# Performance work log

Hardware: AMD Instinct MI355X
Metric: run time of the kernel (lower is better)

## Reference

```python
import jax, jax.numpy as jnp
import numpy as np

WIN = 16
HEADS = 4


def _window_partition(x, win):
    B, H, W, C = x.shape
    x = x.reshape(B, H // win, win, W // win, win, C)
    x = x.transpose(0, 1, 3, 2, 4, 5)
    return x.reshape(-1, win * win, C)


def _reverse_window_partition(x, win, H, W):
    N, _, C = x.shape
    x = x.reshape(-1, H // win, W // win, win, win, C)
    x = x.transpose(0, 1, 3, 2, 4, 5)
    return x.reshape(-1, H, W, C)


def setup_inputs() -> dict:
    key = jax.random.key(0)
    ks = jax.random.split(key, 7)
    B, H, W, C = 2, 256, 256, 96
    s = 0.02
    return {
        "x": jax.random.normal(ks[0], (B, H, W, C), jnp.float32),
        "qkv_w": jax.random.normal(ks[1], (C, 3 * C), jnp.float32) * s,
        "qkv_b": jax.random.normal(ks[2], (3 * C,), jnp.float32) * s,
        "pe_w": jax.random.normal(ks[3], (3, 3, 1, C), jnp.float32) * s,  # depthwise HWIO
        "pe_b": jax.random.normal(ks[4], (C,), jnp.float32) * s,
        "out_w": jax.random.normal(ks[5], (C, C), jnp.float32) * s,
        "out_b": jax.random.normal(ks[6], (C,), jnp.float32) * s,
    }


def reference(x, qkv_w, qkv_b, pe_w, pe_b, out_w, out_b):
    B, H, W, C = x.shape
    win, heads = WIN, HEADS
    hd = C // heads

    z = _window_partition(x, win)
    N, S, _ = z.shape

    qkv = z @ qkv_w + qkv_b                       # (N, S, 3C)
    # headify then chunk(3): each head's 3*hd channels split into q,k,v
    qkv = qkv.reshape(N, S, heads, 3, hd).transpose(0, 2, 3, 1, 4)  # (N, h, 3, S, hd)
    q, k, v = qkv[:, :, 0], qkv[:, :, 1], qkv[:, :, 2]

    # Locally-enhanced PE: depthwise 3x3 conv on de-headified v
    v_img = v.transpose(0, 2, 1, 3).reshape(N, win, win, C)  # NHWC
    lepe = jax.lax.conv_general_dilated(
        v_img, pe_w, (1, 1), 'SAME',
        dimension_numbers=('NHWC', 'HWIO', 'NHWC'),
        feature_group_count=C) + pe_b
    lepe = lepe.reshape(N, S, heads, hd).transpose(0, 2, 1, 3)  # (N, h, S, hd)

    # per-window SDPA (default scale 1/sqrt(hd))
    scale = 1.0 / jnp.sqrt(jnp.asarray(hd, x.dtype))
    attn = jax.nn.softmax(jnp.einsum('nhsd,nhtd->nhst', q, k) * scale, axis=-1)
    o = jnp.einsum('nhst,nhtd->nhsd', attn, v) + lepe

    o = o.transpose(0, 2, 1, 3).reshape(N, S, C)
    o = _reverse_window_partition(o, win, H, W)   # (B, H, W, C)
    return o @ out_w + out_b
```

## Files before the change

### kernel.cpp

```cpp
#include <hip/hip_runtime.h>


typedef __attribute__((ext_vector_type(8))) short bf16x8;
typedef __attribute__((ext_vector_type(4))) float f32x4;

#define MFMA(a, b, c) __builtin_amdgcn_mfma_f32_16x16x32_bf16(a, b, c, 0, 0, 0)

#if __has_builtin(__builtin_amdgcn_exp2f)
#define EXP2F(x) __builtin_amdgcn_exp2f(x)
#else
#define EXP2F(x) exp2f(x)
#endif

#define SCALE2 (0.20412414523193154f * 1.4426950408889634f)

#define OFF_WT   0u
#define OFF_B2   55296u
#define OFF_WTO  56448u
#define OFF_Q    75904u
#define OFF_K    25241728u
#define OFF_VT   50407552u

__device__ __forceinline__ unsigned short f2bf(float f) {
    union { float f; unsigned int u; } v; v.f = f;
    unsigned int u = v.u;
    return (unsigned short)((u + 0x7FFFu + ((u >> 16) & 1u)) >> 16);
}
__device__ __forceinline__ float bf2f(unsigned short h) {
    union { unsigned int u; float f; } v; v.u = ((unsigned int)h) << 16;
    return v.f;
}
__device__ __forceinline__ unsigned int pk2bf(float a, float b) {
#if __has_builtin(__builtin_amdgcn_cvt_pk_bf16_f32)
    auto p = __builtin_amdgcn_cvt_pk_bf16_f32(a, b);
    union { decltype(p) v; unsigned int u; } cv; cv.v = p;
    return cv.u;
#else
    return (unsigned int)f2bf(a) | ((unsigned int)f2bf(b) << 16);
#endif
}
__device__ __forceinline__ float frcp(float x) {
#if __has_builtin(__builtin_amdgcn_rcpf)
    return __builtin_amdgcn_rcpf(x);
#else
    return 1.0f / x;
#endif
}

__global__ void prep_kernel(const float* __restrict__ qkv_w,
                            const float* __restrict__ qkv_b,
                            const float* __restrict__ out_w,
                            unsigned short* __restrict__ wt,
                            float* __restrict__ b2,
                            unsigned short* __restrict__ wto) {
    const int stride = gridDim.x * 256;
    int i0 = blockIdx.x * 256 + threadIdx.x;
    for (int i = i0; i < 288 * 96; i += stride) {
        const int c = i / 96, k = i % 96;
        float v = qkv_w[k * 288 + c];
        if ((c % 72) < 24) v *= SCALE2;
        wt[i] = f2bf(v);
    }
    for (int i = i0; i < 288; i += stride) {
        float v = qkv_b[i];
        if ((i % 72) < 24) v *= SCALE2;
        b2[i] = v;
    }
    for (int i = i0; i < 96 * 96; i += stride) {
        const int c = i / 96, k = i % 96;
        wto[i] = f2bf(out_w[k * 96 + c]);
    }
}

__launch_bounds__(256, 4)
__global__ void qkv_kernel(const float* __restrict__ x,
                           const unsigned short* __restrict__ wt,
                           const float* __restrict__ b2,
                           unsigned short* __restrict__ Qb,
                           unsigned short* __restrict__ Kb,
                           unsigned short* __restrict__ VTb) {
    __shared__ unsigned short z[128 * 104];
    const int blk = blockIdx.x;
    const int n = blk >> 1, half = blk & 1;
    const int T0 = half << 7;
    const int tid = threadIdx.x;
    const int bW = n >> 8, hy = (n >> 4) & 15, wx = n & 15;

    for (int i = tid; i < 128 * 24; i += 256) {
        const int tl = i / 24, c4 = i % 24;
        const int tok = T0 + tl;
        const int y = tok >> 4, xx = tok & 15;
        const size_t row = (size_t)((bW * 256 + hy * 16 + y) * 256 + wx * 16 + xx);
        const float4 v = *(const float4*)(x + row * 96 + c4 * 4);
        uint2 pk; pk.x = pk2bf(v.x, v.y); pk.y = pk2bf(v.z, v.w);
        *(uint2*)&z[tl * 104 + c4 * 4] = pk;
    }
    __syncthreads();

    const int w = tid >> 6, l = tid & 63;
    const int lm = l & 15, lq = l >> 4;

    bf16x8 af[3][3];
#pragma unroll
    for (int mt = 0; mt < 3; mt++)
#pragma unroll
        for (int ks = 0; ks < 3; ks++)
            af[mt][ks] = *(const bf16x8*)(wt + (w * 72 + mt * 16 + lm) * 96 + ks * 32 + lq * 8);

    for (int nt = 0; nt < 8; nt++) {
        bf16x8 bz[3];
#pragma unroll
        for (int ks = 0; ks < 3; ks++)
            bz[ks] = *(const bf16x8*)&z[(nt * 16 + lm) * 104 + ks * 32 + lq * 8];
#pragma unroll
        for (int mt = 0; mt < 3; mt++) {
            f32x4 acc = {0.f, 0.f, 0.f, 0.f};
#pragma unroll
            for (int ks = 0; ks < 3; ks++) acc = MFMA(af[mt][ks], bz[ks], acc);
            const int r48 = mt * 16 + lq * 4;
            const float4 bias = *(const float4*)(b2 + w * 72 + r48);
            const int kind = r48 / 24, idx = r48 % 24;
            const int tok = T0 + nt * 16 + lm;
            uint2 pk;
            pk.x = pk2bf(acc[0] + bias.x, acc[1] + bias.y);
            pk.y = pk2bf(acc[2] + bias.z, acc[3] + bias.w);
            unsigned short* dst = kind ? Kb : Qb;
            *(uint2*)(dst + ((size_t)(n * 4 + w) * 256 + tok) * 24 + idx) = pk;
        }
    }

#pragma unroll
    for (int tt2 = 0; tt2 < 2; tt2++) {
        const int gtt = w * 2 + tt2;
        bf16x8 az[3];
#pragma unroll
        for (int ks = 0; ks < 3; ks++)
            az[ks] = *(const bf16x8*)&z[(gtt * 16 + lm) * 104 + ks * 32 + lq * 8];
#pragma unroll
        for (int nv = 0; nv < 6; nv++) {
            const int j = nv * 16 + lm;
            const int vrow = (j / 24) * 72 + 48 + (j % 24);
            f32x4 acc = {0.f, 0.f, 0.f, 0.f};
#pragma unroll
            for (int ks = 0; ks < 3; ks++) {
                const bf16x8 bw = *(const bf16x8*)(wt + vrow * 96 + ks * 32 + lq * 8);
                acc = MFMA(az[ks], bw, acc);
            }
            const float bv = b2[vrow];
            const int tokb = T0 + gtt * 16 + lq * 4;
            uint2 pk;
            pk.x = pk2bf(acc[0] + bv, acc[1] + bv);
            pk.y = pk2bf(acc[2] + bv, acc[3] + bv);
            *(uint2*)(VTb + ((size_t)(n * 4 + j / 24) * 24 + (j % 24)) * 256 + tokb) = pk;
        }
    }
}

__launch_bounds__(256, 2)
__global__ void attn_out_kernel(const unsigned short* __restrict__ Qb,
                                const unsigned short* __restrict__ Kb,
                                const unsigned short* __restrict__ VTb,
                                const float* __restrict__ pe_w,
                                const float* __restrict__ pe_b,
                                const unsigned short* __restrict__ wto,
                                const float* __restrict__ out_b,
                                float* __restrict__ out) {
    __shared__ unsigned short sVT[32 * 264];
    __shared__ unsigned short sPO[4 * 64 * 40];
    __shared__ float sPW[216];
    __shared__ float sPB[24];

    const int n = blockIdx.x, tid = threadIdx.x;
    const int w = tid >> 6, l = tid & 63;
    const int lm = l & 15, lq = l >> 4;
    const int qbase = w * 64;
    unsigned short* Pw = &sPO[w * 64 * 40];

    f32x4 oacc[4][6];
#pragma unroll
    for (int b = 0; b < 4; b++)
#pragma unroll
        for (int nt = 0; nt < 6; nt++) oacc[b][nt] = (f32x4){0.f, 0.f, 0.f, 0.f};

    for (int h = 0; h < 4; h++) {
        const size_t nh = (size_t)(n * 4 + h);
        __syncthreads();
        for (int i = tid; i < 24 * 64; i += 256) {
            const int row = i >> 6, c = i & 63;
            *(ushort4*)&sVT[row * 264 + c * 4] =
                *(const ushort4*)(VTb + (nh * 24 + row) * 256 + c * 4);
        }
        if (tid < 64) {
            ushort4 ones; ones.x = ones.y = ones.z = ones.w = (unsigned short)0x3F80;
            *(ushort4*)&sVT[24 * 264 + tid * 4] = ones;
        }
        for (int i = tid; i < 216; i += 256) sPW[i] = pe_w[(i / 24) * 96 + h * 24 + (i % 24)];
        if (tid < 24) sPB[tid] = pe_b[h * 24 + tid];

        bf16x8 qf[4];
#pragma unroll
        for (int b = 0; b < 4; b++) {
            bf16x8 qv = *(const bf16x8*)(Qb + (nh * 256 + qbase + b * 16 + lm) * 24 + lq * 8);
            if (lq == 3) qv = (bf16x8)(short)0;
            qf[b] = qv;
        }
        __syncthreads();

        f32x4 oa[4][2];
#pragma unroll
        for (int b = 0; b < 4; b++)
#pragma unroll
            for (int c = 0; c < 2; c++) oa[b][c] = (f32x4){0.f, 0.f, 0.f, 0.f};

        bf16x8 kfn[2];
#pragma unroll
        for (int a = 0; a < 2; a++)
            kfn[a] = *(const bf16x8*)(Kb + (nh * 256 + a * 16 + lm) * 24 + lq * 8);

        for (int kc = 0; kc < 8; kc++) {
            bf16x8 kfc[2] = {kfn[0], kfn[1]};
            if (kc < 7) {
#pragma unroll
                for (int a = 0; a < 2; a++)
                    kfn[a] = *(const bf16x8*)(Kb + (nh * 256 + (kc + 1) * 32 + a * 16 + lm) * 24 + lq * 8);
            }
#pragma unroll
            for (int a = 0; a < 2; a++) {
                f32x4 s[4];
#pragma unroll
                for (int b = 0; b < 4; b++)
                    s[b] = MFMA(kfc[a], qf[b], ((f32x4){0.f, 0.f, 0.f, 0.f}));
#pragma unroll
                for (int b = 0; b < 4; b++) {
                    uint2 pk;
                    pk.x = pk2bf(EXP2F(s[b][0]), EXP2F(s[b][1]));
                    pk.y = pk2bf(EXP2F(s[b][2]), EXP2F(s[b][3]));
                    *(uint2*)&Pw[(b * 16 + lm) * 40 + a * 16 + lq * 4] = pk;
                }
            }
            bf16x8 vb[2];
#pragma unroll
            for (int c = 0; c < 2; c++)
                vb[c] = *(const bf16x8*)&sVT[(c * 16 + lm) * 264 + kc * 32 + lq * 8];
#pragma unroll
            for (int b = 0; b < 4; b++) {
                const bf16x8 pa = *(const bf16x8*)&Pw[(b * 16 + lm) * 40 + lq * 8];
#pragma unroll
                for (int c = 0; c < 2; c++) oa[b][c] = MFMA(pa, vb[c], oa[b][c]);
            }
        }

        {
            uint4 zz = {0u, 0u, 0u, 0u};
            *(uint4*)&Pw[l * 40 + 24] = zz;
        }
        float w9[2][9], pb2[2];
#pragma unroll
        for (int c = 0; c < 2; c++) {
            const int ch = c * 16 + lm;
            if (ch < 24) {
#pragma unroll
                for (int ta = 0; ta < 9; ta++) w9[c][ta] = sPW[ta * 24 + ch];
                pb2[c] = sPB[ch];
            }
        }
#pragma unroll
        for (int b = 0; b < 4; b++) {
            float rinv[4];
#pragma unroll
            for (int r = 0; r < 4; r++)
                rinv[r] = frcp(__shfl(oa[b][1][r], (l & 48) | 8, 64));
            const int y = w * 4 + b;
            const int x0 = lq * 4;
#pragma unroll
            for (int c = 0; c < 2; c++) {
                const int ch = c * 16 + lm;
                if (ch < 24) {
                    float lep[4] = {pb2[c], pb2[c], pb2[c], pb2[c]};
                    const unsigned short* vbase = &sVT[ch * 264];
#pragma unroll
                    for (int dy = -1; dy <= 1; dy++) {
                        const int ny = y + dy;
                        if ((unsigned)ny > 15u) continue;
                        const unsigned short* vrow = vbase + ny * 16;
                        const float wl = w9[c][(dy + 1) * 3 + 0];
                        const float wm = w9[c][(dy + 1) * 3 + 1];
                        const float wr = w9[c][(dy + 1) * 3 + 2];
#pragma unroll
                        for (int d = -1; d <= 4; d++) {
                            const int xx = x0 + d;
                            if ((unsigned)xx > 15u) continue;
                            const float v = bf2f(vrow[xx]);
                            if (d - 1 >= 0 && d - 1 <= 3) lep[d - 1] = fmaf(v, wr, lep[d - 1]);
                            if (d >= 0 && d <= 3)         lep[d]     = fmaf(v, wm, lep[d]);
                            if (d + 1 <= 3)               lep[d + 1] = fmaf(v, wl, lep[d + 1]);
                        }
                    }
#pragma unroll
                    for (int r = 0; r < 4; r++) {
                        const float val = oa[b][c][r] * rinv[r] + lep[r];
                        Pw[(b * 16 + lq * 4 + r) * 40 + ch] = f2bf(val);
                    }
                }
            }
        }

        bf16x8 aO[4];
#pragma unroll
        for (int b = 0; b < 4; b++)
            aO[b] = *(const bf16x8*)&Pw[(b * 16 + lm) * 40 + lq * 8];
#pragma unroll
        for (int nt = 0; nt < 6; nt++) {
            const bf16x8 bwf = *(const bf16x8*)(wto + (nt * 16 + lm) * 96 + h * 24 + lq * 8);
#pragma unroll
            for (int b = 0; b < 4; b++) oacc[b][nt] = MFMA(aO[b], bwf, oacc[b][nt]);
        }
    }

    const int bW = n >> 8, hy = (n >> 4) & 15, wx = n & 15;
#pragma unroll
    for (int nt = 0; nt < 6; nt++) {
        const float bias = out_b[nt * 16 + lm];
#pragma unroll
        for (int b = 0; b < 4; b++) {
#pragma unroll
            for (int r = 0; r < 4; r++) {
                const int t = qbase + b * 16 + lq * 4 + r;
                const size_t grow =
                    (size_t)((bW * 256 + hy * 16 + (t >> 4)) * 256 + wx * 16 + (t & 15));
                out[grow * 96 + nt * 16 + lm] = oacc[b][nt][r] + bias;
            }
        }
    }
}

extern "C" void kernel_launch(void* const* d_in, const int* in_sizes, int n_in,
                              void* d_out, int out_size, void* d_ws, size_t ws_size,
                              hipStream_t stream) {
    const float* x     = (const float*)d_in[0];
    const float* qkv_w = (const float*)d_in[1];
    const float* qkv_b = (const float*)d_in[2];
    const float* pe_w  = (const float*)d_in[3];
    const float* pe_b  = (const float*)d_in[4];
    const float* out_w = (const float*)d_in[5];
    const float* out_b = (const float*)d_in[6];
    float* out = (float*)d_out;

    char* ws = (char*)d_ws;
    unsigned short* wt  = (unsigned short*)(ws + OFF_WT);
    float*          b2  = (float*)(ws + OFF_B2);
    unsigned short* wto = (unsigned short*)(ws + OFF_WTO);
    unsigned short* Qb  = (unsigned short*)(ws + OFF_Q);
    unsigned short* Kb  = (unsigned short*)(ws + OFF_K);
    unsigned short* VTb = (unsigned short*)(ws + OFF_VT);

    prep_kernel<<<72, 256, 0, stream>>>(qkv_w, qkv_b, out_w, wt, b2, wto);
    qkv_kernel<<<1024, 256, 0, stream>>>(x, wt, b2, Qb, Kb, VTb);
    attn_out_kernel<<<512, 256, 0, stream>>>(Qb, Kb, VTb, pe_w, pe_b, wto, out_b, out);
}
```

Before: 200.0 us.

## Fuse QKV projection into attention kernel, keeping Q/K/V in shared memory

Merges the QKV projection and attention/output kernels into one kernel. Each block handles half of a window's queries and recomputes the K and V for the full window per head into LDS, so the bf16 Q/K/V intermediates never go to global memory. This removes the global write and read of the workspace buffers and one launch. In exchange, the K/V projection is computed twice per window (once by each half-block), each block reads the whole window's x, and LDS and register pressure are higher.

```diff
diff --git a/kernel.cpp b/kernel.cpp
--- a/kernel.cpp
+++ b/kernel.cpp
@@ -17,9 +17,6 @@
 #define OFF_WT   0u
 #define OFF_B2   55296u
 #define OFF_WTO  56448u
-#define OFF_Q    75904u
-#define OFF_K    25241728u
-#define OFF_VT   50407552u
 
 __device__ __forceinline__ unsigned short f2bf(float f) {
     union { float f; unsigned int u; } v; v.f = f;
@@ -70,168 +67,179 @@
         const int c = i / 96, k = i % 96;
         wto[i] = f2bf(out_w[k * 96 + c]);
     }
-}
-
-__launch_bounds__(256, 4)
-__global__ void qkv_kernel(const float* __restrict__ x,
-                           const unsigned short* __restrict__ wt,
-                           const float* __restrict__ b2,
-                           unsigned short* __restrict__ Qb,
-                           unsigned short* __restrict__ Kb,
-                           unsigned short* __restrict__ VTb) {
-    __shared__ unsigned short z[128 * 104];
+    for (int i = i0; i < 128; i += stride) wto[96 * 96 + i] = 0;
+}
+
+__launch_bounds__(256, 3)
+__global__ void msa_fused_kernel(const float* __restrict__ x,
+                                 const unsigned short* __restrict__ wt,
+                                 const float* __restrict__ b2,
+                                 const float* __restrict__ pe_w,
+                                 const float* __restrict__ pe_b,
+                                 const unsigned short* __restrict__ wto,
+                                 const float* __restrict__ out_b,
+                                 float* __restrict__ out) {
+    __shared__ __align__(16) unsigned short sK[256 * 24 + 8];
+    __shared__ __align__(16) unsigned short sQ[128 * 24 + 8];
+    __shared__ __align__(16) unsigned short sVT[32 * 264];
+    __shared__ __align__(16) unsigned short sP[4 * 32 * 40];
+    __shared__ __align__(16) float sPW[216];
+    __shared__ __align__(16) float sPB[24];
+
     const int blk = blockIdx.x;
-    const int n = blk >> 1, half = blk & 1;
-    const int T0 = half << 7;
+    const int n = blk >> 1, h2 = blk & 1;
     const int tid = threadIdx.x;
-    const int bW = n >> 8, hy = (n >> 4) & 15, wx = n & 15;
-
-    for (int i = tid; i < 128 * 24; i += 256) {
-        const int tl = i / 24, c4 = i % 24;
-        const int tok = T0 + tl;
-        const int y = tok >> 4, xx = tok & 15;
-        const size_t row = (size_t)((bW * 256 + hy * 16 + y) * 256 + wx * 16 + xx);
-        const float4 v = *(const float4*)(x + row * 96 + c4 * 4);
-        uint2 pk; pk.x = pk2bf(v.x, v.y); pk.y = pk2bf(v.z, v.w);
-        *(uint2*)&z[tl * 104 + c4 * 4] = pk;
-    }
-    __syncthreads();
-
     const int w = tid >> 6, l = tid & 63;
     const int lm = l & 15, lq = l >> 4;
-
-    bf16x8 af[3][3];
-#pragma unroll
-    for (int mt = 0; mt < 3; mt++)
-#pragma unroll
-        for (int ks = 0; ks < 3; ks++)
-            af[mt][ks] = *(const bf16x8*)(wt + (w * 72 + mt * 16 + lm) * 96 + ks * 32 + lq * 8);
-
-    for (int nt = 0; nt < 8; nt++) {
-        bf16x8 bz[3];
-#pragma unroll
-        for (int ks = 0; ks < 3; ks++)
-            bz[ks] = *(const bf16x8*)&z[(nt * 16 + lm) * 104 + ks * 32 + lq * 8];
-#pragma unroll
-        for (int mt = 0; mt < 3; mt++) {
-            f32x4 acc = {0.f, 0.f, 0.f, 0.f};
-#pragma unroll
-            for (int ks = 0; ks < 3; ks++) acc = MFMA(af[mt][ks], bz[ks], acc);
-            const int r48 = mt * 16 + lq * 4;
-            const float4 bias = *(const float4*)(b2 + w * 72 + r48);
-            const int kind = r48 / 24, idx = r48 % 24;
-            const int tok = T0 + nt * 16 + lm;
-            uint2 pk;
-            pk.x = pk2bf(acc[0] + bias.x, acc[1] + bias.y);
-            pk.y = pk2bf(acc[2] + bias.z, acc[3] + bias.w);
-            unsigned short* dst = kind ? Kb : Qb;
-            *(uint2*)(dst + ((size_t)(n * 4 + w) * 256 + tok) * 24 + idx) = pk;
-        }
-    }
-
-#pragma unroll
-    for (int tt2 = 0; tt2 < 2; tt2++) {
-        const int gtt = w * 2 + tt2;
-        bf16x8 az[3];
-#pragma unroll
-        for (int ks = 0; ks < 3; ks++)
-            az[ks] = *(const bf16x8*)&z[(gtt * 16 + lm) * 104 + ks * 32 + lq * 8];
-#pragma unroll
-        for (int nv = 0; nv < 6; nv++) {
-            const int j = nv * 16 + lm;
-            const int vrow = (j / 24) * 72 + 48 + (j % 24);
-            f32x4 acc = {0.f, 0.f, 0.f, 0.f};
-#pragma unroll
-            for (int ks = 0; ks < 3; ks++) {
-                const bf16x8 bw = *(const bf16x8*)(wt + vrow * 96 + ks * 32 + lq * 8);
-                acc = MFMA(az[ks], bw, acc);
-            }
-            const float bv = b2[vrow];
-            const int tokb = T0 + gtt * 16 + lq * 4;
-            uint2 pk;
-            pk.x = pk2bf(acc[0] + bv, acc[1] + bv);
-            pk.y = pk2bf(acc[2] + bv, acc[3] + bv);
-            *(uint2*)(VTb + ((size_t)(n * 4 + j / 24) * 24 + (j % 24)) * 256 + tokb) = pk;
-        }
-    }
-}
-
-__launch_bounds__(256, 2)
-__global__ void attn_out_kernel(const unsigned short* __restrict__ Qb,
-                                const unsigned short* __restrict__ Kb,
-                                const unsigned short* __restrict__ VTb,
-                                const float* __restrict__ pe_w,
-                                const float* __restrict__ pe_b,
-                                const unsigned short* __restrict__ wto,
-                                const float* __restrict__ out_b,
-                                float* __restrict__ out) {
-    __shared__ unsigned short sVT[32 * 264];
-    __shared__ unsigned short sPO[4 * 64 * 40];
-    __shared__ float sPW[216];
-    __shared__ float sPB[24];
-
-    const int n = blockIdx.x, tid = threadIdx.x;
-    const int w = tid >> 6, l = tid & 63;
-    const int lm = l & 15, lq = l >> 4;
-    const int qbase = w * 64;
-    unsigned short* Pw = &sPO[w * 64 * 40];
-
-    f32x4 oacc[4][6];
-#pragma unroll
-    for (int b = 0; b < 4; b++)
+    const int bW = n >> 8, hy = (n >> 4) & 15, wx = n & 15;
+
+    int gtile[4];
+    gtile[0] = h2 * 8 + 2 * w; gtile[1] = gtile[0] + 1;
+    gtile[2] = (1 - h2) * 8 + 2 * w; gtile[3] = gtile[2] + 1;
+
+    if (tid < 8) sK[256 * 24 + tid] = 0;
+    if (tid < 8) sQ[128 * 24 + tid] = 0;
+    for (int i = tid; i < 7 * 132; i += 256)
+        ((unsigned int*)&sVT[25 * 264])[i] = 0u;
+
+    bf16x8 az[4][3];
+#pragma unroll
+    for (int tt = 0; tt < 4; tt++) {
+        const size_t row = (size_t)((bW * 256 + hy * 16 + gtile[tt]) * 256 + wx * 16 + lm);
+#pragma unroll
+        for (int ks = 0; ks < 3; ks++) {
+            const float* p = x + row * 96 + ks * 32 + lq * 8;
+            const float4 f0 = *(const float4*)p;
+            const float4 f1 = *(const float4*)(p + 4);
+            union { bf16x8 v; unsigned int u[4]; } t;
+            t.u[0] = pk2bf(f0.x, f0.y); t.u[1] = pk2bf(f0.z, f0.w);
+            t.u[2] = pk2bf(f1.x, f1.y); t.u[3] = pk2bf(f1.z, f1.w);
+            az[tt][ks] = t.v;
+        }
+    }
+
+    if (tid < 64) {
+        ushort4 ones; ones.x = ones.y = ones.z = ones.w = (unsigned short)0x3F80;
+        *(ushort4*)&sVT[24 * 264 + tid * 4] = ones;
+    }
+
+    f32x4 oacc[2][6];
+#pragma unroll
+    for (int b = 0; b < 2; b++)
 #pragma unroll
         for (int nt = 0; nt < 6; nt++) oacc[b][nt] = (f32x4){0.f, 0.f, 0.f, 0.f};
 
+    unsigned short* Pw = &sP[w * 32 * 40];
+
     for (int h = 0; h < 4; h++) {
-        const size_t nh = (size_t)(n * 4 + h);
         __syncthreads();
-        for (int i = tid; i < 24 * 64; i += 256) {
-            const int row = i >> 6, c = i & 63;
-            *(ushort4*)&sVT[row * 264 + c * 4] =
-                *(const ushort4*)(VTb + (nh * 24 + row) * 256 + c * 4);
-        }
-        if (tid < 64) {
-            ushort4 ones; ones.x = ones.y = ones.z = ones.w = (unsigned short)0x3F80;
-            *(ushort4*)&sVT[24 * 264 + tid * 4] = ones;
-        }
-        for (int i = tid; i < 216; i += 256) sPW[i] = pe_w[(i / 24) * 96 + h * 24 + (i % 24)];
-        if (tid < 24) sPB[tid] = pe_b[h * 24 + tid];
-
-        bf16x8 qf[4];
-#pragma unroll
-        for (int b = 0; b < 4; b++) {
-            bf16x8 qv = *(const bf16x8*)(Qb + (nh * 256 + qbase + b * 16 + lm) * 24 + lq * 8);
+
+        if (tid < 216) sPW[tid] = pe_w[(tid / 24) * 96 + h * 24 + (tid % 24)];
+        if (tid < 24)  sPB[tid] = pe_b[h * 24 + tid];
+
+        {
+            bf16x8 afQ[2][3];
+#pragma unroll
+            for (int mt = 0; mt < 2; mt++)
+#pragma unroll
+                for (int ks = 0; ks < 3; ks++)
+                    afQ[mt][ks] = *(const bf16x8*)(wt + (h * 72 + mt * 16 + lm) * 96 + ks * 32 + lq * 8);
+#pragma unroll
+            for (int tt = 0; tt < 2; tt++) {
+#pragma unroll
+                for (int mt = 0; mt < 2; mt++) {
+                    f32x4 acc = {0.f, 0.f, 0.f, 0.f};
+#pragma unroll
+                    for (int ks = 0; ks < 3; ks++) acc = MFMA(afQ[mt][ks], az[tt][ks], acc);
+                    const int ch0 = mt * 16 + lq * 4;
+                    if (ch0 < 24) {
+                        const float4 bq = *(const float4*)(b2 + h * 72 + ch0);
+                        uint2 pk;
+                        pk.x = pk2bf(acc[0] + bq.x, acc[1] + bq.y);
+                        pk.y = pk2bf(acc[2] + bq.z, acc[3] + bq.w);
+                        *(uint2*)&sQ[(w * 32 + tt * 16 + lm) * 24 + ch0] = pk;
+                    }
+                }
+            }
+        }
+        {
+            bf16x8 afK[2][3];
+#pragma unroll
+            for (int mt = 0; mt < 2; mt++)
+#pragma unroll
+                for (int ks = 0; ks < 3; ks++)
+                    afK[mt][ks] = *(const bf16x8*)(wt + (h * 72 + 24 + mt * 16 + lm) * 96 + ks * 32 + lq * 8);
+#pragma unroll
+            for (int tt = 0; tt < 4; tt++) {
+#pragma unroll
+                for (int mt = 0; mt < 2; mt++) {
+                    f32x4 acc = {0.f, 0.f, 0.f, 0.f};
+#pragma unroll
+                    for (int ks = 0; ks < 3; ks++) acc = MFMA(afK[mt][ks], az[tt][ks], acc);
+                    const int ch0 = mt * 16 + lq * 4;
+                    if (ch0 < 24) {
+                        const float4 bk = *(const float4*)(b2 + h * 72 + 24 + ch0);
+                        uint2 pk;
+                        pk.x = pk2bf(acc[0] + bk.x, acc[1] + bk.y);
+                        pk.y = pk2bf(acc[2] + bk.z, acc[3] + bk.w);
+                        *(uint2*)&sK[(gtile[tt] * 16 + lm) * 24 + ch0] = pk;
+                    }
+                }
+            }
+        }
+        {
+            bf16x8 bv[2][3];
+#pragma unroll
+            for (int vt = 0; vt < 2; vt++)
+#pragma unroll
+                for (int ks = 0; ks < 3; ks++) {
+                    int r = h * 72 + 48 + vt * 16 + lm;
+                    r = r > 287 ? 287 : r;
+                    bv[vt][ks] = *(const bf16x8*)(wt + r * 96 + ks * 32 + lq * 8);
+                }
+#pragma unroll
+            for (int tt = 0; tt < 4; tt++) {
+#pragma unroll
+                for (int vt = 0; vt < 2; vt++) {
+                    f32x4 acc = {0.f, 0.f, 0.f, 0.f};
+#pragma unroll
+                    for (int ks = 0; ks < 3; ks++) acc = MFMA(az[tt][ks], bv[vt][ks], acc);
+                    const int ch = vt * 16 + lm;
+                    if (ch < 24) {
+                        const float bb = b2[h * 72 + 48 + ch];
+                        uint2 pk;
+                        pk.x = pk2bf(acc[0] + bb, acc[1] + bb);
+                        pk.y = pk2bf(acc[2] + bb, acc[3] + bb);
+                        *(uint2*)&sVT[ch * 264 + gtile[tt] * 16 + lq * 4] = pk;
+                    }
+                }
+            }
+        }
+        __syncthreads();
+
+        bf16x8 qf[2];
+#pragma unroll
+        for (int b = 0; b < 2; b++) {
+            bf16x8 qv = *(const bf16x8*)&sQ[(w * 32 + b * 16 + lm) * 24 + lq * 8];
             if (lq == 3) qv = (bf16x8)(short)0;
             qf[b] = qv;
         }
-        __syncthreads();
-
-        f32x4 oa[4][2];
-#pragma unroll
-        for (int b = 0; b < 4; b++)
+        f32x4 oa[2][2];
+#pragma unroll
+        for (int b = 0; b < 2; b++)
 #pragma unroll
             for (int c = 0; c < 2; c++) oa[b][c] = (f32x4){0.f, 0.f, 0.f, 0.f};
 
-        bf16x8 kfn[2];
-#pragma unroll
-        for (int a = 0; a < 2; a++)
-            kfn[a] = *(const bf16x8*)(Kb + (nh * 256 + a * 16 + lm) * 24 + lq * 8);
-
         for (int kc = 0; kc < 8; kc++) {
-            bf16x8 kfc[2] = {kfn[0], kfn[1]};
-            if (kc < 7) {
-#pragma unroll
-                for (int a = 0; a < 2; a++)
-                    kfn[a] = *(const bf16x8*)(Kb + (nh * 256 + (kc + 1) * 32 + a * 16 + lm) * 24 + lq * 8);
-            }
 #pragma unroll
             for (int a = 0; a < 2; a++) {
-                f32x4 s[4];
-#pragma unroll
-                for (int b = 0; b < 4; b++)
-                    s[b] = MFMA(kfc[a], qf[b], ((f32x4){0.f, 0.f, 0.f, 0.f}));
-#pragma unroll
-                for (int b = 0; b < 4; b++) {
+                const bf16x8 kf = *(const bf16x8*)&sK[(kc * 32 + a * 16 + lm) * 24 + lq * 8];
+                f32x4 s[2];
+#pragma unroll
+                for (int b = 0; b < 2; b++)
+                    s[b] = MFMA(kf, qf[b], ((f32x4){0.f, 0.f, 0.f, 0.f}));
+#pragma unroll
+                for (int b = 0; b < 2; b++) {
                     uint2 pk;
                     pk.x = pk2bf(EXP2F(s[b][0]), EXP2F(s[b][1]));
                     pk.y = pk2bf(EXP2F(s[b][2]), EXP2F(s[b][3]));
@@ -243,14 +251,14 @@
             for (int c = 0; c < 2; c++)
                 vb[c] = *(const bf16x8*)&sVT[(c * 16 + lm) * 264 + kc * 32 + lq * 8];
 #pragma unroll
-            for (int b = 0; b < 4; b++) {
+            for (int b = 0; b < 2; b++) {
                 const bf16x8 pa = *(const bf16x8*)&Pw[(b * 16 + lm) * 40 + lq * 8];
 #pragma unroll
                 for (int c = 0; c < 2; c++) oa[b][c] = MFMA(pa, vb[c], oa[b][c]);
             }
         }
 
-        {
+        if (l < 32) {
             uint4 zz = {0u, 0u, 0u, 0u};
             *(uint4*)&Pw[l * 40 + 24] = zz;
         }
@@ -265,12 +273,12 @@
             }
         }
 #pragma unroll
-        for (int b = 0; b < 4; b++) {
+        for (int b = 0; b < 2; b++) {
             float rinv[4];
 #pragma unroll
             for (int r = 0; r < 4; r++)
                 rinv[r] = frcp(__shfl(oa[b][1][r], (l & 48) | 8, 64));
-            const int y = w * 4 + b;
+            const int y = h2 * 8 + 2 * w + b;
             const int x0 = lq * 4;
 #pragma unroll
             for (int c = 0; c < 2; c++) {
@@ -305,27 +313,26 @@
             }
         }
 
-        bf16x8 aO[4];
-#pragma unroll
-        for (int b = 0; b < 4; b++)
+        bf16x8 aO[2];
+#pragma unroll
+        for (int b = 0; b < 2; b++)
             aO[b] = *(const bf16x8*)&Pw[(b * 16 + lm) * 40 + lq * 8];
 #pragma unroll
         for (int nt = 0; nt < 6; nt++) {
             const bf16x8 bwf = *(const bf16x8*)(wto + (nt * 16 + lm) * 96 + h * 24 + lq * 8);
 #pragma unroll
-            for (int b = 0; b < 4; b++) oacc[b][nt] = MFMA(aO[b], bwf, oacc[b][nt]);
-        }
-    }
-
-    const int bW = n >> 8, hy = (n >> 4) & 15, wx = n & 15;
+            for (int b = 0; b < 2; b++) oacc[b][nt] = MFMA(aO[b], bwf, oacc[b][nt]);
+        }
+    }
+
 #pragma unroll
     for (int nt = 0; nt < 6; nt++) {
         const float bias = out_b[nt * 16 + lm];
 #pragma unroll
-        for (int b = 0; b < 4; b++) {
+        for (int b = 0; b < 2; b++) {
 #pragma unroll
             for (int r = 0; r < 4; r++) {
-                const int t = qbase + b * 16 + lq * 4 + r;
+                const int t = h2 * 128 + w * 32 + b * 16 + lq * 4 + r;
                 const size_t grow =
                     (size_t)((bW * 256 + hy * 16 + (t >> 4)) * 256 + wx * 16 + (t & 15));
                 out[grow * 96 + nt * 16 + lm] = oacc[b][nt][r] + bias;
@@ -350,11 +357,7 @@
     unsigned short* wt  = (unsigned short*)(ws + OFF_WT);
     float*          b2  = (float*)(ws + OFF_B2);
     unsigned short* wto = (unsigned short*)(ws + OFF_WTO);
-    unsigned short* Qb  = (unsigned short*)(ws + OFF_Q);
-    unsigned short* Kb  = (unsigned short*)(ws + OFF_K);
-    unsigned short* VTb = (unsigned short*)(ws + OFF_VT);
 
     prep_kernel<<<72, 256, 0, stream>>>(qkv_w, qkv_b, out_w, wt, b2, wto);
-    qkv_kernel<<<1024, 256, 0, stream>>>(x, wt, b2, Qb, Kb, VTb);
-    attn_out_kernel<<<512, 256, 0, stream>>>(Qb, Kb, VTb, pe_w, pe_b, wto, out_b, out);
-}
+    msa_fused_kernel<<<1024, 256, 0, stream>>>(x, wt, b2, pe_w, pe_b, wto, out_b, out);
+}
```

Result: slower. 302.0 us (+51.0%).
